# Kernel tuning notes

Measured on AMD Instinct MI355X. Metric: run time of the kernel, lower is better.

Reference implementation:

```python
import jax, jax.numpy as jnp
import numpy as np
from itertools import combinations

# 2-source PID on the redundancy lattice (Williams-Beer), antichains indexed
# over sources {0,1}; index 2 is the output variable axis.
FULL = (0, 1, 2)
ANTICHAINS = [((0,), (1,)), ((0,),), ((1,),), ((0, 1),)]  # red, unq0, unq1, syn (cumulative I)
MOEBIUS = np.array([[1, 0, 0, 0],
                    [-1, 1, 0, 0],
                    [-1, 0, 1, 0],
                    [1, -1, -1, 1]], dtype=np.float32)
EPS_DEN = 1e-10
EPS_FRAC = 1e-7


def _marginals(p):
    """Powerset marginals of the joint p over axes (0,1,2); trailing axis = neurons."""
    m = {}
    for r in range(1, 4):
        for a in combinations(FULL, r):
            ax = tuple(sorted(set(FULL) - set(a)))
            m[a] = p.sum(ax, keepdims=True) if ax else p
    return m


def _union(m, alpha):
    """Inclusion-exclusion union probability over the sets in antichain alpha."""
    res = 0.0
    for k in range(1, len(alpha) + 1):
        for beta in combinations(alpha, k):
            b_union = tuple(sorted({b for a in beta for b in a}))
            res = res + ((-1) ** (k - 1)) * m[b_union]
    return res


def _isx(m, alpha, p_full):
    """I_cap^sx for one antichain: sum over joint of p * log2 ratio."""
    p_union = jax.lax.stop_gradient(_union(m, alpha))            # no_grad in original
    alpha_t = tuple(tuple(sorted(a + (2,))) for a in alpha)       # append output var
    p_union_t = _union(m, alpha_t)
    frac = p_union_t / (p_union * m[(2,)] + EPS_DEN)
    frac = jnp.where(frac < EPS_FRAC, jnp.asarray(1.0, frac.dtype), frac)
    return (p_full * jnp.log2(frac)).sum((0, 1, 2))               # -> (N,)


def _pid(p):
    m = _marginals(p)
    I_cap = jnp.stack([_isx(m, a, p) for a in ANTICHAINS])        # (4, N)
    Pi = jnp.asarray(MOEBIUS, p.dtype) @ I_cap                    # Moebius transform (4, N)
    p_out = m[(2,)]                                               # (1, 1, out_bins, N)
    H_tot = -(p_out * jnp.log2(p_out + EPS_DEN)).sum(-2)          # (1, 1, N)
    H_res = (H_tot - I_cap[ANTICHAINS.index(((0, 1),))]).reshape(-1)
    return jnp.concatenate([Pi, H_res[None]], axis=0)             # (5, N): red,unq0,unq1,syn,H_res


def setup_inputs() -> dict:
    key = jax.random.key(0)
    # joint histogram over (src1_bins=16, src2_bins=16, out_bins=2, n_neurons=100000)
    p = jax.random.uniform(key, (16, 16, 2, 100000), dtype=jnp.float32)
    p = p / p.sum((0, 1, 2), keepdims=True)  # normalize to a distribution per neuron
    return {"p_all_neurons": p}


def reference(p_all_neurons):
    return _pid(p_all_neurons)
```

## Files before the change

### kernel.cpp

```cpp
#include <hip/hip_runtime.h>

#define LOG2_EPS_CLAMP -23.2534966f

__device__ __forceinline__ float flog2(float x) { return __builtin_amdgcn_logf(x); }

__global__ __launch_bounds__(256) void pid_kernel(const float* __restrict__ p,
                                                  float* __restrict__ out,
                                                  const int N) {
    __shared__ float m12buf[32][64];
    __shared__ float ibuf[3][4][64];

    const int tid = threadIdx.x;
    const int g   = tid & 63;
    const int s   = tid >> 6;
    const int n   = blockIdx.x * 64 + g;
    const bool active = (n < N);

    #pragma unroll
    for (int t = 0; t < 8; ++t) ((float*)m12buf)[t * 256 + tid] = 0.f;
    __syncthreads();

    const float* __restrict__ q = p + n;

    float a0[4], a1[4];
    float part[32];
    #pragma unroll
    for (int t = 0; t < 32; ++t) part[t] = 0.f;

    if (active) {
        #pragma unroll
        for (int ii = 0; ii < 4; ++ii) {
            const int i = s * 4 + ii;
            const float* __restrict__ qi = q + (size_t)(i * 32) * (size_t)N;
            float s0 = 0.f, s1 = 0.f;
            #pragma unroll
            for (int j = 0; j < 16; ++j) {
                const float f0 = qi[(size_t)(2 * j) * (size_t)N];
                const float f1 = qi[(size_t)(2 * j + 1) * (size_t)N];
                s0 += f0; s1 += f1;
                part[2 * j]     += f0;
                part[2 * j + 1] += f1;
            }
            a0[ii] = s0; a1[ii] = s1;
        }
        #pragma unroll
        for (int t = 0; t < 32; ++t) atomicAdd(&m12buf[t][g], part[t]);
    }
    __syncthreads();

    float m12[32];
    #pragma unroll
    for (int t = 0; t < 32; ++t) m12[t] = m12buf[t][g];

    float P20 = 0.f, P21 = 0.f;
    #pragma unroll
    for (int j = 0; j < 16; ++j) { P20 += m12[2 * j]; P21 += m12[2 * j + 1]; }
    const float LP20 = flog2(P20);
    const float LP21 = flog2(P21);

    float I1 = 0.f, I2 = 0.f, I4 = 0.f;
    if (active) {
        #pragma unroll
        for (int ii = 0; ii < 4; ++ii) {
            const int i = s * 4 + ii;
            const float a0i = a0[ii], a1i = a1[ii];
            const float m0i = a0i + a1i;
            const float* __restrict__ qi = q + (size_t)(i * 32) * (size_t)N;
            #pragma unroll
            for (int j = 0; j < 16; ++j) {
                const float f0  = qi[(size_t)(2 * j) * (size_t)N];
                const float f1  = qi[(size_t)(2 * j + 1) * (size_t)N];
                const float p01 = f0 + f1;
                const float m1j = m12[2 * j] + m12[2 * j + 1];
                const float u1  = m0i + m1j - p01;
                const float Lu1  = flog2(u1);
                const float Lp01 = flog2(p01);
                {
                    const float num = a0i + m12[2 * j] - f0;
                    float l1 = flog2(num) - Lu1 - LP20;
                    l1 = (l1 < LOG2_EPS_CLAMP) ? 0.f : l1;
                    I1 = fmaf(f0, l1, I1);
                    float l4 = flog2(f0) - Lp01 - LP20;
                    l4 = (l4 < LOG2_EPS_CLAMP) ? 0.f : l4;
                    I4 = fmaf(f0, l4, I4);
                }
                {
                    const float num = a1i + m12[2 * j + 1] - f1;
                    float l1 = flog2(num) - Lu1 - LP21;
                    l1 = (l1 < LOG2_EPS_CLAMP) ? 0.f : l1;
                    I1 = fmaf(f1, l1, I1);
                    float l4 = flog2(f1) - Lp01 - LP21;
                    l4 = (l4 < LOG2_EPS_CLAMP) ? 0.f : l4;
                    I4 = fmaf(f1, l4, I4);
                }
            }
            const float L0 = flog2(m0i);
            float la = flog2(a0i) - L0 - LP20;
            la = (la < LOG2_EPS_CLAMP) ? 0.f : la;
            I2 = fmaf(a0i, la, I2);
            float lb = flog2(a1i) - L0 - LP21;
            lb = (lb < LOG2_EPS_CLAMP) ? 0.f : lb;
            I2 = fmaf(a1i, lb, I2);
        }
    }
    ibuf[0][s][g] = I1;
    ibuf[1][s][g] = I2;
    ibuf[2][s][g] = I4;
    __syncthreads();

    if (s == 0 && active) {
        I1 = ibuf[0][0][g] + ibuf[0][1][g] + ibuf[0][2][g] + ibuf[0][3][g];
        I2 = ibuf[1][0][g] + ibuf[1][1][g] + ibuf[1][2][g] + ibuf[1][3][g];
        I4 = ibuf[2][0][g] + ibuf[2][1][g] + ibuf[2][2][g] + ibuf[2][3][g];

        float I3 = 0.f;
        #pragma unroll
        for (int j = 0; j < 16; ++j) {
            const float L1 = flog2(m12[2 * j] + m12[2 * j + 1]);
            float la = flog2(m12[2 * j]) - L1 - LP20;
            la = (la < LOG2_EPS_CLAMP) ? 0.f : la;
            I3 = fmaf(m12[2 * j], la, I3);
            float lb = flog2(m12[2 * j + 1]) - L1 - LP21;
            lb = (lb < LOG2_EPS_CLAMP) ? 0.f : lb;
            I3 = fmaf(m12[2 * j + 1], lb, I3);
        }
        const float H = -(P20 * flog2(P20 + 1e-10f) + P21 * flog2(P21 + 1e-10f));

        out[0 * N + n] = I1;
        out[1 * N + n] = I2 - I1;
        out[2 * N + n] = I3 - I1;
        out[3 * N + n] = I1 - I2 - I3 + I4;
        out[4 * N + n] = H - I4;
    }
}

extern "C" void kernel_launch(void* const* d_in, const int* in_sizes, int n_in,
                              void* d_out, int out_size, void* d_ws, size_t ws_size,
                              hipStream_t stream) {
    const float* p = (const float*)d_in[0];
    float* out = (float*)d_out;
    const int N = in_sizes[0] / 512;
    const int blocks = (N + 63) / 64;
    pid_kernel<<<blocks, 256, 0, stream>>>(p, out, N);
}
```

Baseline: 340.2 us.

## Keep input slice in registers and double threads per block to avoid re-reading global memory

The kernel previously read each input element from global memory twice: once to build marginals and again in the log pass. Now each of 8 waves loads its 2 rows (32 values each) into registers once and reuses them for the log computation. Block size doubles to 512 so each wave handles fewer rows, and per-column marginals are read from LDS instead of being cached in a 32-register array. This removes the second global read pass at the cost of more LDS reads and a larger block-level reduction.

```diff
diff --git a/kernel.cpp b/kernel.cpp
--- a/kernel.cpp
+++ b/kernel.cpp
@@ -4,11 +4,11 @@
 
 __device__ __forceinline__ float flog2(float x) { return __builtin_amdgcn_logf(x); }
 
-__global__ __launch_bounds__(256) void pid_kernel(const float* __restrict__ p,
+__global__ __launch_bounds__(512) void pid_kernel(const float* __restrict__ p,
                                                   float* __restrict__ out,
                                                   const int N) {
     __shared__ float m12buf[32][64];
-    __shared__ float ibuf[3][4][64];
+    __shared__ float ibuf[3][8][64];
 
     const int tid = threadIdx.x;
     const int g   = tid & 63;
@@ -17,91 +17,91 @@
     const bool active = (n < N);
 
     #pragma unroll
-    for (int t = 0; t < 8; ++t) ((float*)m12buf)[t * 256 + tid] = 0.f;
+    for (int t = 0; t < 4; ++t) ((float*)m12buf)[t * 512 + tid] = 0.f;
     __syncthreads();
 
     const float* __restrict__ q = p + n;
 
-    float a0[4], a1[4];
-    float part[32];
-    #pragma unroll
-    for (int t = 0; t < 32; ++t) part[t] = 0.f;
-
+    float f0a[2][16], f1a[2][16];
     if (active) {
         #pragma unroll
-        for (int ii = 0; ii < 4; ++ii) {
-            const int i = s * 4 + ii;
-            const float* __restrict__ qi = q + (size_t)(i * 32) * (size_t)N;
-            float s0 = 0.f, s1 = 0.f;
+        for (int ii = 0; ii < 2; ++ii) {
+            const float* __restrict__ qi = q + (size_t)((2 * s + ii) * 32) * (size_t)N;
             #pragma unroll
             for (int j = 0; j < 16; ++j) {
-                const float f0 = qi[(size_t)(2 * j) * (size_t)N];
-                const float f1 = qi[(size_t)(2 * j + 1) * (size_t)N];
-                s0 += f0; s1 += f1;
-                part[2 * j]     += f0;
-                part[2 * j + 1] += f1;
+                f0a[ii][j] = qi[(size_t)(2 * j) * (size_t)N];
+                f1a[ii][j] = qi[(size_t)(2 * j + 1) * (size_t)N];
             }
-            a0[ii] = s0; a1[ii] = s1;
         }
         #pragma unroll
-        for (int t = 0; t < 32; ++t) atomicAdd(&m12buf[t][g], part[t]);
+        for (int j = 0; j < 16; ++j) {
+            atomicAdd(&m12buf[2 * j][g],     f0a[0][j] + f0a[1][j]);
+            atomicAdd(&m12buf[2 * j + 1][g], f1a[0][j] + f1a[1][j]);
+        }
+    } else {
+        #pragma unroll
+        for (int ii = 0; ii < 2; ++ii)
+            #pragma unroll
+            for (int j = 0; j < 16; ++j) { f0a[ii][j] = 0.f; f1a[ii][j] = 0.f; }
     }
     __syncthreads();
 
-    float m12[32];
-    #pragma unroll
-    for (int t = 0; t < 32; ++t) m12[t] = m12buf[t][g];
-
     float P20 = 0.f, P21 = 0.f;
     #pragma unroll
-    for (int j = 0; j < 16; ++j) { P20 += m12[2 * j]; P21 += m12[2 * j + 1]; }
+    for (int j = 0; j < 16; ++j) { P20 += m12buf[2 * j][g]; P21 += m12buf[2 * j + 1][g]; }
     const float LP20 = flog2(P20);
     const float LP21 = flog2(P21);
 
+    float a0[2], a1[2];
+    #pragma unroll
+    for (int ii = 0; ii < 2; ++ii) {
+        float s0 = 0.f, s1 = 0.f;
+        #pragma unroll
+        for (int j = 0; j < 16; ++j) { s0 += f0a[ii][j]; s1 += f1a[ii][j]; }
+        a0[ii] = s0; a1[ii] = s1;
+    }
+
     float I1 = 0.f, I2 = 0.f, I4 = 0.f;
-    if (active) {
+    #pragma unroll
+    for (int ii = 0; ii < 2; ++ii) {
+        const float a0i = a0[ii], a1i = a1[ii];
+        const float m0i = a0i + a1i;
         #pragma unroll
-        for (int ii = 0; ii < 4; ++ii) {
-            const int i = s * 4 + ii;
-            const float a0i = a0[ii], a1i = a1[ii];
-            const float m0i = a0i + a1i;
-            const float* __restrict__ qi = q + (size_t)(i * 32) * (size_t)N;
-            #pragma unroll
-            for (int j = 0; j < 16; ++j) {
-                const float f0  = qi[(size_t)(2 * j) * (size_t)N];
-                const float f1  = qi[(size_t)(2 * j + 1) * (size_t)N];
-                const float p01 = f0 + f1;
-                const float m1j = m12[2 * j] + m12[2 * j + 1];
-                const float u1  = m0i + m1j - p01;
-                const float Lu1  = flog2(u1);
-                const float Lp01 = flog2(p01);
-                {
-                    const float num = a0i + m12[2 * j] - f0;
-                    float l1 = flog2(num) - Lu1 - LP20;
-                    l1 = (l1 < LOG2_EPS_CLAMP) ? 0.f : l1;
-                    I1 = fmaf(f0, l1, I1);
-                    float l4 = flog2(f0) - Lp01 - LP20;
-                    l4 = (l4 < LOG2_EPS_CLAMP) ? 0.f : l4;
-                    I4 = fmaf(f0, l4, I4);
-                }
-                {
-                    const float num = a1i + m12[2 * j + 1] - f1;
-                    float l1 = flog2(num) - Lu1 - LP21;
-                    l1 = (l1 < LOG2_EPS_CLAMP) ? 0.f : l1;
-                    I1 = fmaf(f1, l1, I1);
-                    float l4 = flog2(f1) - Lp01 - LP21;
-                    l4 = (l4 < LOG2_EPS_CLAMP) ? 0.f : l4;
-                    I4 = fmaf(f1, l4, I4);
-                }
+        for (int j = 0; j < 16; ++j) {
+            const float w0 = m12buf[2 * j][g];
+            const float w1 = m12buf[2 * j + 1][g];
+            const float f0  = f0a[ii][j];
+            const float f1  = f1a[ii][j];
+            const float p01 = f0 + f1;
+            const float u1  = m0i + (w0 + w1) - p01;
+            const float Lu1  = flog2(u1);
+            const float Lp01 = flog2(p01);
+            {
+                const float num = a0i + w0 - f0;
+                float l1 = flog2(num) - Lu1 - LP20;
+                l1 = (l1 < LOG2_EPS_CLAMP) ? 0.f : l1;
+                I1 = fmaf(f0, l1, I1);
+                float l4 = flog2(f0) - Lp01 - LP20;
+                l4 = (l4 < LOG2_EPS_CLAMP) ? 0.f : l4;
+                I4 = fmaf(f0, l4, I4);
             }
-            const float L0 = flog2(m0i);
-            float la = flog2(a0i) - L0 - LP20;
-            la = (la < LOG2_EPS_CLAMP) ? 0.f : la;
-            I2 = fmaf(a0i, la, I2);
-            float lb = flog2(a1i) - L0 - LP21;
-            lb = (lb < LOG2_EPS_CLAMP) ? 0.f : lb;
-            I2 = fmaf(a1i, lb, I2);
+            {
+                const float num = a1i + w1 - f1;
+                float l1 = flog2(num) - Lu1 - LP21;
+                l1 = (l1 < LOG2_EPS_CLAMP) ? 0.f : l1;
+                I1 = fmaf(f1, l1, I1);
+                float l4 = flog2(f1) - Lp01 - LP21;
+                l4 = (l4 < LOG2_EPS_CLAMP) ? 0.f : l4;
+                I4 = fmaf(f1, l4, I4);
+            }
         }
+        const float L0 = flog2(m0i);
+        float la = flog2(a0i) - L0 - LP20;
+        la = (la < LOG2_EPS_CLAMP) ? 0.f : la;
+        I2 = fmaf(a0i, la, I2);
+        float lb = flog2(a1i) - L0 - LP21;
+        lb = (lb < LOG2_EPS_CLAMP) ? 0.f : lb;
+        I2 = fmaf(a1i, lb, I2);
     }
     ibuf[0][s][g] = I1;
     ibuf[1][s][g] = I2;
@@ -109,28 +109,34 @@
     __syncthreads();
 
     if (s == 0 && active) {
-        I1 = ibuf[0][0][g] + ibuf[0][1][g] + ibuf[0][2][g] + ibuf[0][3][g];
-        I2 = ibuf[1][0][g] + ibuf[1][1][g] + ibuf[1][2][g] + ibuf[1][3][g];
-        I4 = ibuf[2][0][g] + ibuf[2][1][g] + ibuf[2][2][g] + ibuf[2][3][g];
+        float r1 = 0.f, r2 = 0.f, r4 = 0.f;
+        #pragma unroll
+        for (int w = 0; w < 8; ++w) {
+            r1 += ibuf[0][w][g];
+            r2 += ibuf[1][w][g];
+            r4 += ibuf[2][w][g];
+        }
 
         float I3 = 0.f;
         #pragma unroll
         for (int j = 0; j < 16; ++j) {
-            const float L1 = flog2(m12[2 * j] + m12[2 * j + 1]);
-            float la = flog2(m12[2 * j]) - L1 - LP20;
+            const float w0 = m12buf[2 * j][g];
+            const float w1 = m12buf[2 * j + 1][g];
+            const float L1 = flog2(w0 + w1);
+            float la = flog2(w0) - L1 - LP20;
             la = (la < LOG2_EPS_CLAMP) ? 0.f : la;
-            I3 = fmaf(m12[2 * j], la, I3);
-            float lb = flog2(m12[2 * j + 1]) - L1 - LP21;
+            I3 = fmaf(w0, la, I3);
+            float lb = flog2(w1) - L1 - LP21;
             lb = (lb < LOG2_EPS_CLAMP) ? 0.f : lb;
-            I3 = fmaf(m12[2 * j + 1], lb, I3);
+            I3 = fmaf(w1, lb, I3);
         }
         const float H = -(P20 * flog2(P20 + 1e-10f) + P21 * flog2(P21 + 1e-10f));
 
-        out[0 * N + n] = I1;
-        out[1 * N + n] = I2 - I1;
-        out[2 * N + n] = I3 - I1;
-        out[3 * N + n] = I1 - I2 - I3 + I4;
-        out[4 * N + n] = H - I4;
+        out[0 * N + n] = r1;
+        out[1 * N + n] = r2 - r1;
+        out[2 * N + n] = I3 - r1;
+        out[3 * N + n] = r1 - r2 - I3 + r4;
+        out[4 * N + n] = H - r4;
     }
 }
 
@@ -141,5 +147,5 @@
     float* out = (float*)d_out;
     const int N = in_sizes[0] / 512;
     const int blocks = (N + 63) / 64;
-    pid_kernel<<<blocks, 256, 0, stream>>>(p, out, N);
+    pid_kernel<<<blocks, 512, 0, stream>>>(p, out, N);
 }
```

After: 366.5 us. +7.7%, slower.
